# Optimization experiments

Measured on AMD Instinct MI355X. Metric: run time of the kernel, lower is better.

The kernel has to match this reference:

```python
import jax, jax.numpy as jnp
import numpy as np
import math

B, D = 4096, 2048  # batch, input_size == hidden_size


def setup_inputs() -> dict:
    key = jax.random.key(0)
    ks = jax.random.split(key, 9)
    stdv = 1.0 / math.sqrt(D)
    u = lambda k, shp: jax.random.uniform(k, shp, jnp.float32, -stdv, stdv)
    return {
        "inputs": jax.random.normal(ks[0], (B, D), jnp.float32),
        "frac_n": jax.random.normal(ks[1], (B, D), jnp.float32),
        "frac_d": jax.random.uniform(ks[2], (B, D), jnp.float32, 0.1, 1.0),
        "scale": jax.random.normal(ks[3], (B, D), jnp.float32),
        "w_r": u(ks[4], (D, D)),
        "w_k": u(ks[5], (D, D)),
        "w_v": u(ks[6], (D, D)),
        "w_o": u(ks[7], (D, D)),
        "w_u": jnp.ones((D,), jnp.float32),  # init.ones_ for 1-D params
        "w_w": jnp.ones((D,), jnp.float32),
    }


def reference(inputs, frac_n, frac_d, scale, w_r, w_k, w_v, w_o, w_u, w_w):
    # r/k/v projections: [B,D] @ [D,D]^T
    r_t = jax.nn.sigmoid(inputs @ w_r.T)
    k_t = inputs @ w_k.T
    v_t = inputs @ w_v.T

    # stabilized WKV update (output path, includes bonus w_u)
    softmax_scale = jnp.maximum(scale, w_u + k_t)
    cell_mult = jnp.exp(scale - softmax_scale)
    attn_mult = jnp.exp(w_u + k_t - softmax_scale)
    frac_n_t = cell_mult * frac_n + attn_mult * v_t
    frac_d_t = cell_mult * frac_d + attn_mult

    # state update path (decay w_w, no bonus)
    next_scale = jnp.maximum(scale + w_w, k_t)
    next_cell_mult = jnp.exp(scale + w_w - next_scale)
    next_attn_mult = jnp.exp(k_t - next_scale)
    next_frac_n = next_cell_mult * frac_n + next_attn_mult * v_t
    next_frac_d = next_cell_mult * frac_d + next_attn_mult

    output = (r_t * (frac_n_t / frac_d_t)) @ w_o.T
    return (output, next_frac_n, next_frac_d, next_scale)
```

## Files before the change

kernel.cpp:

```cpp
#include <hip/hip_runtime.h>
#include <hip/hip_bf16.h>
#include <stdint.h>

#define B_SZ 4096
#define D_SZ 2048

typedef __attribute__((ext_vector_type(4))) float f32x4;
typedef __attribute__((ext_vector_type(8))) __bf16 bf16x8;
typedef __attribute__((ext_vector_type(4))) unsigned short u16x4;
typedef unsigned short u16;

static constexpr long BD = (long)B_SZ * D_SZ;
static constexpr long DD = (long)D_SZ * D_SZ;

__device__ __forceinline__ u16 f2bf(float f) {
  union { float f; unsigned int u; } c; c.f = f;
  unsigned int u = c.u;
  u = (u + 0x7fffu + ((u >> 16) & 1u)) >> 16;
  return (u16)u;
}
__device__ __forceinline__ float bf2f(u16 h) {
  union { unsigned int u; float f; } c; c.u = ((unsigned int)h) << 16;
  return c.f;
}

__global__ __launch_bounds__(256) void k_convert(
    const float* __restrict__ x,  const float* __restrict__ wr,
    const float* __restrict__ wk, const float* __restrict__ wv,
    const float* __restrict__ wo,
    u16* __restrict__ Xb, u16* __restrict__ W3b, u16* __restrict__ Wob) {
  long i = ((long)blockIdx.x * 256 + threadIdx.x) * 4;
  const float* src; u16* dst; long so, dofs;
  if (i < BD)               { src = x;  so = i;            dst = Xb;  dofs = so; }
  else if (i < BD + DD)     { src = wr; so = i - BD;       dst = W3b; dofs = i - BD; }
  else if (i < BD + 2*DD)   { src = wk; so = i - BD - DD;  dst = W3b; dofs = i - BD; }
  else if (i < BD + 3*DD)   { src = wv; so = i - BD - 2*DD; dst = W3b; dofs = i - BD; }
  else                      { src = wo; so = i - BD - 3*DD; dst = Wob; dofs = so; }
  f32x4 v = *reinterpret_cast<const f32x4*>(src + so);
  u16x4 o;
  o[0] = f2bf(v[0]); o[1] = f2bf(v[1]); o[2] = f2bf(v[2]); o[3] = f2bf(v[3]);
  *reinterpret_cast<u16x4*>(dst + dofs) = o;
}

__device__ __forceinline__ void gload16(const u16* g, const u16* l) {
  __builtin_amdgcn_global_load_lds(
      (const __attribute__((address_space(1))) unsigned int*)g,
      (__attribute__((address_space(3))) unsigned int*)l, 16, 0, 0);
}

#define FENCE asm volatile("" ::: "memory")
#define BAR do { FENCE; __builtin_amdgcn_s_barrier(); FENCE; } while (0)
#define VMC(n) asm volatile("s_waitcnt vmcnt(" #n ")" ::: "memory")

__global__ __launch_bounds__(256, 2) void k_fused(
    const u16* __restrict__ A, const u16* __restrict__ W3,
    const float* __restrict__ frac_n, const float* __restrict__ frac_d,
    const float* __restrict__ scale,
    const float* __restrict__ w_u, const float* __restrict__ w_w,
    float* __restrict__ o_nfn, float* __restrict__ o_nfd,
    float* __restrict__ o_ns,  u16* __restrict__ ab) {
  __shared__ __align__(16) u16 lds[40960];
  const int tid = threadIdx.x;
  const int l   = tid & 63;
  const int w   = tid >> 6;
  const int wm  = w >> 1, wn = w & 1;
  const int bm = blockIdx.y, bn = blockIdx.x;
  const int K  = D_SZ;
  const int NT = K >> 6;

  const int gcol = (((l & 7) ^ (l >> 3)) << 3);
  const u16* Abase = A  + (long)(bm * 128 + w * 32 + (l >> 3)) * K + gcol;
  const u16* Rbase = W3 +          (long)(bn * 64 + w * 16 + (l >> 3)) * K + gcol;
  const u16* Kbase = W3 + DD     + (long)(bn * 64 + w * 16 + (l >> 3)) * K + gcol;
  const u16* Vbase = W3 + 2 * DD + (long)(bn * 64 + w * 16 + (l >> 3)) * K + gcol;
  const int Asd = w * 2048;
  const int Bsd = w * 1024;

  #define STAGE(t) do {                                                  \
    const long _ko = (long)(t) * 64;                                     \
    u16* _buf = &lds[((t) & 1) * 20480];                                 \
    _Pragma("unroll")                                                    \
    for (int _c = 0; _c < 4; ++_c)                                       \
      gload16(Abase + (long)_c * 8 * K + _ko, _buf + Asd + _c * 512);    \
    _Pragma("unroll")                                                    \
    for (int _c = 0; _c < 2; ++_c) {                                     \
      gload16(Rbase + (long)_c * 8 * K + _ko, _buf +  8192 + Bsd + _c * 512); \
      gload16(Kbase + (long)_c * 8 * K + _ko, _buf + 12288 + Bsd + _c * 512); \
      gload16(Vbase + (long)_c * 8 * K + _ko, _buf + 16384 + Bsd + _c * 512); \
    }                                                                    \
  } while (0)

  const int rby  = (l & 15) * 128;
  const int obx0 = ((l >> 4) * 16) ^ ((l & 7) << 4);
  const int lo0  = (rby + obx0) >> 1;
  const int lo1  = lo0 ^ 32;

  f32x4 acc[3][4][2] = {};

  auto COMPUTE = [&](int p) {
    const int base = p * 20480;
#pragma unroll
    for (int ks = 0; ks < 2; ++ks) {
      const int lo = ks ? lo1 : lo0;
      bf16x8 af[4], fb[3][2];
#pragma unroll
      for (int mi = 0; mi < 4; ++mi)
        af[mi] = *reinterpret_cast<const bf16x8*>(
            &lds[base + (wm * 4 + mi) * 1024 + lo]);
#pragma unroll
      for (int j = 0; j < 3; ++j)
#pragma unroll
        for (int ni = 0; ni < 2; ++ni)
          fb[j][ni] = *reinterpret_cast<const bf16x8*>(
              &lds[base + 8192 + j * 4096 + (wn * 2 + ni) * 1024 + lo]);
      __builtin_amdgcn_s_setprio(1);
#pragma unroll
      for (int j = 0; j < 3; ++j)
#pragma unroll
        for (int mi = 0; mi < 4; ++mi)
#pragma unroll
          for (int ni = 0; ni < 2; ++ni)
            acc[j][mi][ni] = __builtin_amdgcn_mfma_f32_16x16x32_bf16(
                af[mi], fb[j][ni], acc[j][mi][ni], 0, 0, 0);
      __builtin_amdgcn_s_setprio(0);
    }
  };

  STAGE(0);
  VMC(0); BAR;
  for (int t = 0; t < NT - 1; ++t) {
    STAGE(t + 1);
    COMPUTE(t & 1);
    VMC(0); BAR;
  }
  COMPUTE((NT - 1) & 1);
  #undef STAGE

  const int rb = (l >> 4) * 4, cb = l & 15;
  const long row0 = (long)bm * 128 + wm * 64 + rb;
  const long col0 = (long)bn * 64 + wn * 32 + cb;
#pragma unroll
  for (int mi = 0; mi < 4; ++mi)
#pragma unroll
    for (int ni = 0; ni < 2; ++ni) {
      const long gc  = col0 + ni * 16;
      const float wuv = w_u[gc];
      const float wwv = w_w[gc];
#pragma unroll
      for (int r = 0; r < 4; ++r) {
        const long gr  = row0 + mi * 16 + r;
        const long idx = gr * D_SZ + gc;
        const float rr = acc[0][mi][ni][r];
        const float kk = acc[1][mi][ni][r];
        const float vv = acc[2][mi][ni][r];
        const float n  = frac_n[idx];
        const float dn = frac_d[idx];
        const float s  = scale[idx];

        const float rt  = 1.0f / (1.0f + __expf(-rr));
        const float ss  = fmaxf(s, wuv + kk);
        const float cm  = __expf(s - ss);
        const float am  = __expf(wuv + kk - ss);
        const float fnt = cm * n + am * vv;
        const float fdt = cm * dn + am;

        const float ns2 = fmaxf(s + wwv, kk);
        const float ncm = __expf(s + wwv - ns2);
        const float nam = __expf(kk - ns2);

        o_nfn[idx] = ncm * n + nam * vv;
        o_nfd[idx] = ncm * dn + nam;
        o_ns[idx]  = ns2;
        ab[idx]    = f2bf(rt * (fnt / fdt));
      }
    }
}

template <bool OUT_BF16>
__global__ __launch_bounds__(256, 4) void k_gemm128(
    const u16* __restrict__ A, const u16* __restrict__ Bm,
    void* __restrict__ C, int M, int N, int K) {
  __shared__ __align__(16) u16 lds[32768];
  const int tid = threadIdx.x;
  const int l   = tid & 63;
  const int w   = tid >> 6;
  const int wm  = w >> 1, wn = w & 1;
  const int bm = blockIdx.y, bn = blockIdx.x;
  const int NT = K >> 6;

  const int gcol  = (((l & 7) ^ (l >> 3)) << 3);
  const int grow  = w * 32 + (l >> 3);
  const u16* Abase = A  + (long)(bm * 128 + grow) * K + gcol;
  const u16* Bbase = Bm + (long)(bn * 128 + grow) * K + gcol;
  const int sdst = w * 2048;

  #define STAGE(t) do {                                              \
    const long _ko = (long)(t) * 64;                                 \
    u16* _da = &lds[((t) & 1) * 16384 + sdst];                       \
    u16* _db = _da + 8192;                                           \
    _Pragma("unroll")                                                \
    for (int _c = 0; _c < 4; ++_c) {                                 \
      gload16(Abase + (long)_c * 8 * K + _ko, _da + _c * 512);       \
      gload16(Bbase + (long)_c * 8 * K + _ko, _db + _c * 512);       \
    }                                                                \
  } while (0)

  const int rby  = (l & 15) * 128;
  const int obx0 = ((l >> 4) * 16) ^ ((l & 7) << 4);
  const int lo0  = (rby + obx0) >> 1;
  const int lo1  = lo0 ^ 32;

  f32x4 acc[4][4] = {};

  auto COMPUTE = [&](int p) {
#pragma unroll
    for (int ks = 0; ks < 2; ++ks) {
      const int lo = ks ? lo1 : lo0;
      bf16x8 af[4], bf[4];
#pragma unroll
      for (int mi = 0; mi < 4; ++mi)
        af[mi] = *reinterpret_cast<const bf16x8*>(
            &lds[p * 16384 + (wm * 4 + mi) * 1024 + lo]);
#pragma unroll
      for (int ni = 0; ni < 4; ++ni)
        bf[ni] = *reinterpret_cast<const bf16x8*>(
            &lds[p * 16384 + 8192 + (wn * 4 + ni) * 1024 + lo]);
      __builtin_amdgcn_s_setprio(1);
#pragma unroll
      for (int mi = 0; mi < 4; ++mi)
#pragma unroll
        for (int ni = 0; ni < 4; ++ni)
          acc[mi][ni] = __builtin_amdgcn_mfma_f32_16x16x32_bf16(
              af[mi], bf[ni], acc[mi][ni], 0, 0, 0);
      __builtin_amdgcn_s_setprio(0);
    }
  };

  STAGE(0);
  VMC(0); BAR;
  for (int t = 0; t < NT - 1; ++t) {
    STAGE(t + 1);
    COMPUTE(t & 1);
    VMC(0); BAR;
  }
  COMPUTE((NT - 1) & 1);
  #undef STAGE

  const int rb = (l >> 4) * 4, cb = l & 15;
  const long Crow0 = (long)bm * 128 + wm * 64 + rb;
  const long Ccol0 = (long)bn * 128 + wn * 64 + cb;
#pragma unroll
  for (int mi = 0; mi < 4; ++mi)
#pragma unroll
    for (int ni = 0; ni < 4; ++ni)
#pragma unroll
      for (int r = 0; r < 4; ++r) {
        const long gr = Crow0 + mi * 16 + r;
        const long gc = Ccol0 + ni * 16;
        if constexpr (OUT_BF16)
          ((u16*)C)[gr * N + gc] = f2bf(acc[mi][ni][r]);
        else
          ((float*)C)[gr * N + gc] = acc[mi][ni][r];
      }
}

extern "C" void kernel_launch(void* const* d_in, const int* in_sizes, int n_in,
                              void* d_out, int out_size, void* d_ws, size_t ws_size,
                              hipStream_t stream) {
  const float* x      = (const float*)d_in[0];
  const float* frac_n = (const float*)d_in[1];
  const float* frac_d = (const float*)d_in[2];
  const float* scale  = (const float*)d_in[3];
  const float* wr     = (const float*)d_in[4];
  const float* wk     = (const float*)d_in[5];
  const float* wv     = (const float*)d_in[6];
  const float* wo     = (const float*)d_in[7];
  const float* wu     = (const float*)d_in[8];
  const float* ww     = (const float*)d_in[9];
  float* out = (float*)d_out;

  u16* Xb   = (u16*)d_ws;
  u16* W3b  = Xb + BD;
  u16* Wob  = W3b + 3 * DD;
  u16* ab   = Wob + DD;

  {
    const long total = BD + 4 * DD;
    const int blocks = (int)(total / 4 / 256);
    k_convert<<<blocks, 256, 0, stream>>>(x, wr, wk, wv, wo, Xb, W3b, Wob);
  }
  k_fused<<<dim3(D_SZ / 64, B_SZ / 128), 256, 0, stream>>>(
      Xb, W3b, frac_n, frac_d, scale, wu, ww,
      out + BD, out + 2 * BD, out + 3 * BD, ab);
  k_gemm128<false><<<dim3(D_SZ / 128, B_SZ / 128), 256, 0, stream>>>(
      ab, Wob, out, B_SZ, D_SZ, D_SZ);
}
```

Baseline: 203.0 us.

## Split fused RKV GEMM block across eight waves to cut per-wave accumulators

```diff
diff --git a/kernel.cpp b/kernel.cpp
--- a/kernel.cpp
+++ b/kernel.cpp
@@ -18,10 +18,6 @@
   unsigned int u = c.u;
   u = (u + 0x7fffu + ((u >> 16) & 1u)) >> 16;
   return (u16)u;
-}
-__device__ __forceinline__ float bf2f(u16 h) {
-  union { unsigned int u; float f; } c; c.u = ((unsigned int)h) << 16;
-  return c.f;
 }
 
 __global__ __launch_bounds__(256) void k_convert(
@@ -52,7 +48,7 @@
 #define BAR do { FENCE; __builtin_amdgcn_s_barrier(); FENCE; } while (0)
 #define VMC(n) asm volatile("s_waitcnt vmcnt(" #n ")" ::: "memory")
 
-__global__ __launch_bounds__(256, 2) void k_fused(
+__global__ __launch_bounds__(512, 4) void k_fused(
     const u16* __restrict__ A, const u16* __restrict__ W3,
     const float* __restrict__ frac_n, const float* __restrict__ frac_d,
     const float* __restrict__ scale,
@@ -62,32 +58,29 @@
   __shared__ __align__(16) u16 lds[40960];
   const int tid = threadIdx.x;
   const int l   = tid & 63;
-  const int w   = tid >> 6;
-  const int wm  = w >> 1, wn = w & 1;
+  const int wid = tid >> 6;
+  const int wm  = wid >> 2;
+  const int wn  = wid & 3;
   const int bm = blockIdx.y, bn = blockIdx.x;
   const int K  = D_SZ;
   const int NT = K >> 6;
 
   const int gcol = (((l & 7) ^ (l >> 3)) << 3);
-  const u16* Abase = A  + (long)(bm * 128 + w * 32 + (l >> 3)) * K + gcol;
-  const u16* Rbase = W3 +          (long)(bn * 64 + w * 16 + (l >> 3)) * K + gcol;
-  const u16* Kbase = W3 + DD     + (long)(bn * 64 + w * 16 + (l >> 3)) * K + gcol;
-  const u16* Vbase = W3 + 2 * DD + (long)(bn * 64 + w * 16 + (l >> 3)) * K + gcol;
-  const int Asd = w * 2048;
-  const int Bsd = w * 1024;
-
-  #define STAGE(t) do {                                                  \
-    const long _ko = (long)(t) * 64;                                     \
-    u16* _buf = &lds[((t) & 1) * 20480];                                 \
-    _Pragma("unroll")                                                    \
-    for (int _c = 0; _c < 4; ++_c)                                       \
-      gload16(Abase + (long)_c * 8 * K + _ko, _buf + Asd + _c * 512);    \
-    _Pragma("unroll")                                                    \
-    for (int _c = 0; _c < 2; ++_c) {                                     \
-      gload16(Rbase + (long)_c * 8 * K + _ko, _buf +  8192 + Bsd + _c * 512); \
-      gload16(Kbase + (long)_c * 8 * K + _ko, _buf + 12288 + Bsd + _c * 512); \
-      gload16(Vbase + (long)_c * 8 * K + _ko, _buf + 16384 + Bsd + _c * 512); \
-    }                                                                    \
+  const u16* Abase = A + (long)(bm * 128 + wid * 16 + (l >> 3)) * K + gcol;
+  const int i0 = wid * 3;
+
+  #define STAGE(t) do {                                                        \
+    const long _ko = (long)(t) * 64;                                           \
+    u16* _b = &lds[((t) & 1) * 20480];                                         \
+    gload16(Abase + _ko,                _b + wid * 1024);                      \
+    gload16(Abase + 8 * (long)K + _ko,  _b + wid * 1024 + 512);                \
+    _Pragma("unroll")                                                          \
+    for (int _c = 0; _c < 3; ++_c) {                                           \
+      const int _i = i0 + _c, _j = _i >> 3, _rc = _i & 7;                      \
+      const u16* _g = W3 + (long)_j * DD                                       \
+                    + (long)(bn * 64 + _rc * 8 + (l >> 3)) * K + gcol + _ko;   \
+      gload16(_g, _b + 8192 + _j * 4096 + _rc * 512);                          \
+    }                                                                          \
   } while (0)
 
   const int rby  = (l & 15) * 128;
@@ -95,33 +88,29 @@
   const int lo0  = (rby + obx0) >> 1;
   const int lo1  = lo0 ^ 32;
 
-  f32x4 acc[3][4][2] = {};
+  f32x4 acc[3][4] = {};
 
   auto COMPUTE = [&](int p) {
     const int base = p * 20480;
 #pragma unroll
     for (int ks = 0; ks < 2; ++ks) {
       const int lo = ks ? lo1 : lo0;
-      bf16x8 af[4], fb[3][2];
+      bf16x8 af[4], fb[3];
 #pragma unroll
       for (int mi = 0; mi < 4; ++mi)
         af[mi] = *reinterpret_cast<const bf16x8*>(
-            &lds[base + (wm * 4 + mi) * 1024 + lo]);
+            &lds[base + wm * 4096 + mi * 1024 + lo]);
 #pragma unroll
       for (int j = 0; j < 3; ++j)
-#pragma unroll
-        for (int ni = 0; ni < 2; ++ni)
-          fb[j][ni] = *reinterpret_cast<const bf16x8*>(
-              &lds[base + 8192 + j * 4096 + (wn * 2 + ni) * 1024 + lo]);
+        fb[j] = *reinterpret_cast<const bf16x8*>(
+            &lds[base + 8192 + j * 4096 + wn * 1024 + lo]);
       __builtin_amdgcn_s_setprio(1);
 #pragma unroll
       for (int j = 0; j < 3; ++j)
 #pragma unroll
         for (int mi = 0; mi < 4; ++mi)
-#pragma unroll
-          for (int ni = 0; ni < 2; ++ni)
-            acc[j][mi][ni] = __builtin_amdgcn_mfma_f32_16x16x32_bf16(
-                af[mi], fb[j][ni], acc[j][mi][ni], 0, 0, 0);
+          acc[j][mi] = __builtin_amdgcn_mfma_f32_16x16x32_bf16(
+              af[mi], fb[j], acc[j][mi], 0, 0, 0);
       __builtin_amdgcn_s_setprio(0);
     }
   };
@@ -136,43 +125,38 @@
   COMPUTE((NT - 1) & 1);
   #undef STAGE
 
-  const int rb = (l >> 4) * 4, cb = l & 15;
-  const long row0 = (long)bm * 128 + wm * 64 + rb;
-  const long col0 = (long)bn * 64 + wn * 32 + cb;
+  const long row0 = (long)bm * 128 + wm * 64 + (l >> 4) * 4;
+  const long gc   = (long)bn * 64 + wn * 16 + (l & 15);
+  const float wuv = w_u[gc];
+  const float wwv = w_w[gc];
 #pragma unroll
   for (int mi = 0; mi < 4; ++mi)
 #pragma unroll
-    for (int ni = 0; ni < 2; ++ni) {
-      const long gc  = col0 + ni * 16;
-      const float wuv = w_u[gc];
-      const float wwv = w_w[gc];
-#pragma unroll
-      for (int r = 0; r < 4; ++r) {
-        const long gr  = row0 + mi * 16 + r;
-        const long idx = gr * D_SZ + gc;
-        const float rr = acc[0][mi][ni][r];
-        const float kk = acc[1][mi][ni][r];
-        const float vv = acc[2][mi][ni][r];
-        const float n  = frac_n[idx];
-        const float dn = frac_d[idx];
-        const float s  = scale[idx];
-
-        const float rt  = 1.0f / (1.0f + __expf(-rr));
-        const float ss  = fmaxf(s, wuv + kk);
-        const float cm  = __expf(s - ss);
-        const float am  = __expf(wuv + kk - ss);
-        const float fnt = cm * n + am * vv;
-        const float fdt = cm * dn + am;
-
-        const float ns2 = fmaxf(s + wwv, kk);
-        const float ncm = __expf(s + wwv - ns2);
-        const float nam = __expf(kk - ns2);
-
-        o_nfn[idx] = ncm * n + nam * vv;
-        o_nfd[idx] = ncm * dn + nam;
-        o_ns[idx]  = ns2;
-        ab[idx]    = f2bf(rt * (fnt / fdt));
-      }
+    for (int r = 0; r < 4; ++r) {
+      const long gr  = row0 + mi * 16 + r;
+      const long idx = gr * D_SZ + gc;
+      const float rr = acc[0][mi][r];
+      const float kk = acc[1][mi][r];
+      const float vv = acc[2][mi][r];
+      const float n  = frac_n[idx];
+      const float dn = frac_d[idx];
+      const float s  = scale[idx];
+
+      const float rt  = 1.0f / (1.0f + __expf(-rr));
+      const float ss  = fmaxf(s, wuv + kk);
+      const float cm  = __expf(s - ss);
+      const float am  = __expf(wuv + kk - ss);
+      const float fnt = cm * n + am * vv;
+      const float fdt = cm * dn + am;
+
+      const float ns2 = fmaxf(s + wwv, kk);
+      const float ncm = __expf(s + wwv - ns2);
+      const float nam = __expf(kk - ns2);
+
+      o_nfn[idx] = ncm * n + nam * vv;
+      o_nfd[idx] = ncm * dn + nam;
+      o_ns[idx]  = ns2;
+      ab[idx]    = f2bf(rt * (fnt / fdt));
     }
 }
 
@@ -289,7 +273,7 @@
     const int blocks = (int)(total / 4 / 256);
     k_convert<<<blocks, 256, 0, stream>>>(x, wr, wk, wv, wo, Xb, W3b, Wob);
   }
-  k_fused<<<dim3(D_SZ / 64, B_SZ / 128), 256, 0, stream>>>(
+  k_fused<<<dim3(D_SZ / 64, B_SZ / 128), 512, 0, stream>>>(
       Xb, W3b, frac_n, frac_d, scale, wu, ww,
       out + BD, out + 2 * BD, out + 3 * BD, ab);
   k_gemm128<false><<<dim3(D_SZ / 128, B_SZ / 128), 256, 0, stream>>>(
```

Result: faster. 198.7 us, median of 3 (-2.1%).
